# Performance work log

Measured on AMD Instinct MI355X. Metric: run time of the kernel, lower is better.

Reference implementation:

```python
import jax, jax.numpy as jnp
import numpy as np

N, H, W, C = 8, 64, 64, 256  # C//4 = 64 query channels, HW = 4096 attention size


def setup_inputs() -> dict:
    key = jax.random.key(0)
    k1, k2, k3, k4 = jax.random.split(key, 4)
    src_mask = jax.random.uniform(k1, (N, H, W), dtype=jnp.float32)
    src_feature = jax.random.normal(k2, (N, H, W, C), dtype=jnp.float32)
    ref_feature = jax.random.normal(k3, (N, H, W, C), dtype=jnp.float32)
    w_query = jax.random.normal(k4, (C, C // 4), dtype=jnp.float32) * 0.02  # 1x1 conv weight
    return {"src_mask": src_mask, "src_feature": src_feature,
            "ref_feature": ref_feature, "w_query": w_query}


def _apply_attention_map(att_map, features):
    n, h, w, c = features.shape
    pixels = features.reshape(n, h * w, c).transpose(0, 2, 1)  # (N, C, HW)
    att_out = jnp.einsum('ncp,npq->ncq', pixels, att_map)      # (N, C, HW)
    return att_out.reshape(n, h, w, c)


def reference(src_mask, src_feature, ref_feature, w_query):
    n, h, w, c = src_feature.shape
    # 1x1 conv (no bias): per-pixel channel projection C -> C//4
    query = jnp.einsum('nhwc,cd->nhwd', src_feature, w_query).reshape(n, h * w, -1)
    # full (HW x HW) attention map, softmax over keys
    att_map = jax.nn.softmax(jnp.einsum('npd,nqd->npq', query, query), axis=-1)
    # original module applies the map to src_feature twice (src_att and ref_att)
    att_out = _apply_attention_map(att_map, src_feature)
    src_att = att_out
    ref_att = att_out
    m = src_mask[..., None]  # (N, H, W, 1)
    ex_guide_flow = m * ref_att + (1.0 - m) * ref_feature
    return jnp.concatenate([ex_guide_flow, src_att], axis=-1)  # (N, H, W, 2C)
```

## Files before the change

kernel.cpp:

```cpp
#include <hip/hip_runtime.h>

typedef unsigned short u16;
typedef unsigned int u32;
typedef __attribute__((ext_vector_type(8))) __bf16 bf16x8;
typedef __attribute__((ext_vector_type(8))) _Float16 f16x8;
typedef __attribute__((ext_vector_type(4))) float f32x4;

__device__ __forceinline__ float b2f(u16 b) {
    union { u32 u; float f; } v; v.u = ((u32)b) << 16; return v.f;
}
__device__ __forceinline__ u16 f2bf(float f) {
    union { float f; u32 u; } v; v.f = f;
    u32 u = v.u;
    return (u16)((u + 0x7fffu + ((u >> 16) & 1u)) >> 16);
}
__device__ __forceinline__ u16 f2h(float f) {
    _Float16 h = (_Float16)f;
    return __builtin_bit_cast(u16, h);
}
__device__ __forceinline__ u32 pkbf2(float a, float b) {
    u16 x = __builtin_bit_cast(u16, (__bf16)a);
    u16 y = __builtin_bit_cast(u16, (__bf16)b);
    return (u32)x | ((u32)y << 16);
}
__device__ __forceinline__ bf16x8 ldg8b(const u16* p) {
    uint4 v = *(const uint4*)p;
    return __builtin_bit_cast(bf16x8, v);
}
__device__ __forceinline__ f16x8 ldg8h(const u16* p) {
    uint4 v = *(const uint4*)p;
    return __builtin_bit_cast(f16x8, v);
}
__device__ __forceinline__ f32x4 mfma_bf(bf16x8 a, bf16x8 b, f32x4 c) {
    return __builtin_amdgcn_mfma_f32_16x16x32_bf16(a, b, c, 0, 0, 0);
}
__device__ __forceinline__ f32x4 mfma_h(f16x8 a, f16x8 b, f32x4 c) {
    return __builtin_amdgcn_mfma_f32_16x16x32_f16(a, b, c, 0, 0, 0);
}
__device__ __forceinline__ void gld16(const u16* g, u16* l) {
    __builtin_amdgcn_global_load_lds(
        (const __attribute__((address_space(1))) u32*)g,
        (__attribute__((address_space(3))) u32*)l, 16, 0, 0);
}

#define LOG2E 1.44269504088896340736f


__global__ void k0_wt(const float* __restrict__ Wq,
                      u16* __restrict__ Wthi, u16* __restrict__ Wtlo) {
    int idx = blockIdx.x * 256 + threadIdx.x;
    int c = idx >> 6, d = idx & 63;
    float w = Wq[idx];
    u16 hi = f2bf(w);
    float rem = w - b2f(hi);
    Wthi[d * 256 + c] = hi;
    Wtlo[d * 256 + c] = f2bf(rem);
}

__global__ __launch_bounds__(256) void k1_query(
    const float* __restrict__ F, const u16* __restrict__ Wthi,
    const u16* __restrict__ Wtlo, u16* __restrict__ Qh) {
    const int t = threadIdx.x;
    const int w = t >> 6, L = t & 63, lane16 = L & 15, quad = L >> 4;
    const int R0 = blockIdx.x * 64;
    const int row = R0 + w * 16 + lane16;
    const f32x4 z4 = {0.f, 0.f, 0.f, 0.f};
    f32x4 acc[4] = {z4, z4, z4, z4};
    union U8 { bf16x8 v; u16 s[8]; };
#pragma unroll
    for (int ks = 0; ks < 8; ++ks) {
        const float* fp = F + (size_t)row * 256 + ks * 32 + quad * 8;
        float4 x0 = *(const float4*)fp;
        float4 x1 = *(const float4*)(fp + 4);
        float xs[8] = {x0.x, x0.y, x0.z, x0.w, x1.x, x1.y, x1.z, x1.w};
        U8 ahi, alo;
#pragma unroll
        for (int j = 0; j < 8; ++j) {
            u16 h = f2bf(xs[j]);
            ahi.s[j] = h;
            alo.s[j] = f2bf(xs[j] - b2f(h));
        }
#pragma unroll
        for (int nt = 0; nt < 4; ++nt) {
            const int off = (nt * 16 + lane16) * 256 + ks * 32 + quad * 8;
            bf16x8 bh = ldg8b(Wthi + off);
            bf16x8 bl = ldg8b(Wtlo + off);
            acc[nt] = mfma_bf(ahi.v, bh, acc[nt]);
            acc[nt] = mfma_bf(alo.v, bh, acc[nt]);
            acc[nt] = mfma_bf(ahi.v, bl, acc[nt]);
        }
    }
    const int orow = R0 + w * 16 + quad * 4;
#pragma unroll
    for (int nt = 0; nt < 4; ++nt) {
        const int d = nt * 16 + lane16;
#pragma unroll
        for (int r = 0; r < 4; ++r) {
            const int p = orow + r;
            Qh[(size_t)p * 64 + (d ^ ((p & 7) << 3))] = f2h(acc[nt][r]);
        }
    }
}

__global__ __launch_bounds__(256) void k2_suminv(
    const u16* __restrict__ Q, float* __restrict__ lgl) {
    const int t = threadIdx.x;
    const int w = t >> 6, L = t & 63, lane16 = L & 15, quad = L >> 4, l7 = lane16 & 7;
    const int bx = blockIdx.x;
    const int n = bx & 7, pb = bx >> 3;
    const int P0 = pb * 32;
    const u16* Qn = Q + (size_t)n * 4096 * 64;

    f16x8 ap[2][2];
#pragma unroll
    for (int st = 0; st < 2; ++st) {
        const int row = P0 + st * 16 + lane16;
        ap[st][0] = ldg8h(Qn + row * 64 + ((quad * 8) ^ (l7 * 8)));
        ap[st][1] = ldg8h(Qn + row * 64 + ((32 + quad * 8) ^ (l7 * 8)));
    }
    float sums[2][4];
#pragma unroll
    for (int st = 0; st < 2; ++st)
#pragma unroll
        for (int r = 0; r < 4; ++r) sums[st][r] = 0.f;

    const f32x4 z4 = {0.f, 0.f, 0.f, 0.f};
    for (int s = 0; s < 32; ++s) {
#pragma unroll
        for (int nt = 0; nt < 2; ++nt) {
            const int qr = w * 1024 + s * 32 + nt * 16 + lane16;
            f16x8 b0 = ldg8h(Qn + qr * 64 + ((quad * 8) ^ (l7 * 8)));
            f16x8 b1 = ldg8h(Qn + qr * 64 + ((32 + quad * 8) ^ (l7 * 8)));
#pragma unroll
            for (int st = 0; st < 2; ++st) {
                f32x4 z = z4;
                z = mfma_h(ap[st][0], b0, z);
                z = mfma_h(ap[st][1], b1, z);
                sums[st][0] += __expf(z[0]);
                sums[st][1] += __expf(z[1]);
                sums[st][2] += __expf(z[2]);
                sums[st][3] += __expf(z[3]);
            }
        }
    }
    __shared__ float red[4][32];
#pragma unroll
    for (int st = 0; st < 2; ++st)
#pragma unroll
        for (int r = 0; r < 4; ++r) {
            float v = sums[st][r];
            v += __shfl_xor(v, 1);
            v += __shfl_xor(v, 2);
            v += __shfl_xor(v, 4);
            v += __shfl_xor(v, 8);
            if (lane16 == 0) red[w][st * 16 + quad * 4 + r] = v;
        }
    __syncthreads();
    if (t < 32) {
        float tot = red[0][t] + red[1][t] + red[2][t] + red[3][t];
        lgl[n * 4096 + P0 + t] = -__log2f(tot);
    }
}

__global__ __launch_bounds__(256) void k3_gt(
    const float* __restrict__ F, u16* __restrict__ Gt) {
    const int t = threadIdx.x;
    const int bx = blockIdx.x;
    const int n = bx >> 6, s = bx & 63;
    const int p0 = s * 64;
    __shared__ float tile[64][65];
    const float* Fn = F + (size_t)n * 4096 * 256;
    u16* Gn = Gt + (size_t)(n * 64 + s) * 16384;
#pragma unroll 1
    for (int ct = 0; ct < 4; ++ct) {
        const int c0 = ct * 64;
        if (ct > 0) __syncthreads();
#pragma unroll
        for (int k = 0; k < 16; ++k) {
            int idx = k * 256 + t;
            int r = idx >> 6, cc = idx & 63;
            tile[r][cc] = Fn[(size_t)(p0 + r) * 256 + c0 + cc];
        }
        __syncthreads();
#pragma unroll
        for (int k = 0; k < 2; ++k) {
            int u = k * 256 + t;
            int cc = u & 63, S = u >> 6;
            int G = S ^ (cc & 7);
            u16 v[8];
#pragma unroll
            for (int j = 0; j < 8; ++j) v[j] = f2bf(tile[G * 8 + j][cc]);
            uint4 pk;
            pk.x = (u32)v[0] | ((u32)v[1] << 16);
            pk.y = (u32)v[2] | ((u32)v[3] << 16);
            pk.z = (u32)v[4] | ((u32)v[5] << 16);
            pk.w = (u32)v[6] | ((u32)v[7] << 16);
            *(uint4*)&Gn[(c0 + cc) * 64 + S * 8] = pk;
        }
    }
}

__global__ __launch_bounds__(256, 2) void k4_attn(
    const u16* __restrict__ Q, const u16* __restrict__ Gt,
    const float* __restrict__ lgl, const float* __restrict__ mask,
    const float* __restrict__ ref, float* __restrict__ out) {
    const int t = threadIdx.x;
    const int w = t >> 6, L = t & 63, lane16 = L & 15, quad = L >> 4, l7 = lane16 & 7;
    const int bx = blockIdx.x;
    const int n = bx & 7, qb = bx >> 3;
    const int q0 = qb << 6;

    __shared__ u16 sGt[2][16384];
    __shared__ u16 sP[2][4096];

    const u16* Qn = Q + (size_t)n * 4096 * 64;
    const u16* Gtn = Gt + (size_t)n * 64 * 16384;
    const float* iln = lgl + n * 4096;

    f16x8 bq[4][2];
#pragma unroll
    for (int qt = 0; qt < 4; ++qt) {
        const int row = q0 + qt * 16 + lane16;
        bq[qt][0] = ldg8h(Qn + row * 64 + ((quad * 8) ^ (l7 * 8)));
        bq[qt][1] = ldg8h(Qn + row * 64 + ((32 + quad * 8) ^ (l7 * 8)));
    }

    const int sAg0 = (w * 16 + lane16) * 64 + ((quad * 8) ^ (l7 * 8));
    const int sAg1 = (w * 16 + lane16) * 64 + ((32 + quad * 8) ^ (l7 * 8));
    int wrP[4];
#pragma unroll
    for (int qt = 0; qt < 4; ++qt)
        wrP[qt] = (qt * 16 + lane16) * 64 +
                  ((w * 16 + 8 * (quad >> 1)) ^ (l7 * 8)) + 4 * (quad & 1);
    int rdP[4][2], sOf[4][2];
#pragma unroll
    for (int m = 0; m < 4; ++m)
#pragma unroll
        for (int h = 0; h < 2; ++h)
            rdP[m][h] = (m * 16 + lane16) * 64 + ((h * 32 + quad * 8) ^ (l7 * 8));
#pragma unroll
    for (int nt = 0; nt < 4; ++nt)
#pragma unroll
        for (int h = 0; h < 2; ++h)
            sOf[nt][h] = (w * 64 + nt * 16 + lane16) * 64 + ((h * 32 + quad * 8) ^ (l7 * 8));
    const int dl = L * 8;

    const f32x4 z4 = {0.f, 0.f, 0.f, 0.f};
    f32x4 acc[4][4];
#pragma unroll
    for (int a = 0; a < 4; ++a)
#pragma unroll
        for (int b = 0; b < 4; ++b) acc[a][b] = z4;

    {
        f16x8 a0 = ldg8h(Qn + sAg0);
        f16x8 a1 = ldg8h(Qn + sAg1);
        float4 il4 = *(const float4*)(iln + w * 16 + quad * 4);
        float lg[4] = {il4.x, il4.y, il4.z, il4.w};
#pragma unroll
        for (int qt = 0; qt < 4; ++qt) {
            f32x4 z = z4;
            z = mfma_h(a0, bq[qt][0], z);
            z = mfma_h(a1, bq[qt][1], z);
            uint2 pk;
            pk.x = pkbf2(__builtin_exp2f(__builtin_fmaf(z[0], LOG2E, lg[0])),
                         __builtin_exp2f(__builtin_fmaf(z[1], LOG2E, lg[1])));
            pk.y = pkbf2(__builtin_exp2f(__builtin_fmaf(z[2], LOG2E, lg[2])),
                         __builtin_exp2f(__builtin_fmaf(z[3], LOG2E, lg[3])));
            *(uint2*)&sP[0][wrP[qt]] = pk;
        }
    }
    __builtin_amdgcn_sched_barrier(0);
#pragma unroll
    for (int j = 0; j < 8; ++j) {
        const int c = w * 8 + j;
        gld16(Gtn + c * 512 + dl, &sGt[0][c * 512]);
    }
    __builtin_amdgcn_sched_barrier(0);
    f16x8 na0 = ldg8h(Qn + 4096 + sAg0);
    f16x8 na1 = ldg8h(Qn + 4096 + sAg1);
    float4 nil4 = *(const float4*)(iln + 64 + w * 16 + quad * 4);
    __builtin_amdgcn_sched_barrier(0);
    asm volatile("s_waitcnt lgkmcnt(0)" ::: "memory");
    __builtin_amdgcn_s_barrier();

#pragma unroll 1
    for (int i = 0; i < 64; ++i) {
        const int cur = i & 1, nxt = cur ^ 1;
        if (i + 1 < 64) {
            float lg[4] = {nil4.x, nil4.y, nil4.z, nil4.w};
#pragma unroll
            for (int qt = 0; qt < 4; ++qt) {
                f32x4 z = z4;
                z = mfma_h(na0, bq[qt][0], z);
                z = mfma_h(na1, bq[qt][1], z);
                uint2 pk;
                pk.x = pkbf2(__builtin_exp2f(__builtin_fmaf(z[0], LOG2E, lg[0])),
                             __builtin_exp2f(__builtin_fmaf(z[1], LOG2E, lg[1])));
                pk.y = pkbf2(__builtin_exp2f(__builtin_fmaf(z[2], LOG2E, lg[2])),
                             __builtin_exp2f(__builtin_fmaf(z[3], LOG2E, lg[3])));
                *(uint2*)&sP[nxt][wrP[qt]] = pk;
            }
            __builtin_amdgcn_sched_barrier(0);
            const u16* gsrc = Gtn + (size_t)(i + 1) * 16384;
#pragma unroll
            for (int j = 0; j < 8; ++j) {
                const int c = w * 8 + j;
                gld16(gsrc + c * 512 + dl, &sGt[nxt][c * 512]);
            }
            __builtin_amdgcn_sched_barrier(0);
            if (i + 2 < 64) {
                na0 = ldg8h(Qn + (size_t)(i + 2) * 4096 + sAg0);
                na1 = ldg8h(Qn + (size_t)(i + 2) * 4096 + sAg1);
                nil4 = *(const float4*)(iln + (i + 2) * 64 + w * 16 + quad * 4);
            }
            __builtin_amdgcn_sched_barrier(0);
        } else {
            asm volatile("s_waitcnt vmcnt(0)" ::: "memory");
        }
#pragma unroll
        for (int h = 0; h < 2; ++h) {
            bf16x8 af[4], bb[4];
#pragma unroll
            for (int m = 0; m < 4; ++m) af[m] = ldg8b(&sP[cur][rdP[m][h]]);
#pragma unroll
            for (int nt = 0; nt < 4; ++nt) bb[nt] = ldg8b(&sGt[cur][sOf[nt][h]]);
#pragma unroll
            for (int nt = 0; nt < 4; ++nt)
#pragma unroll
                for (int m = 0; m < 4; ++m)
                    acc[m][nt] = mfma_bf(af[m], bb[nt], acc[m][nt]);
        }
        asm volatile("s_waitcnt lgkmcnt(0)" ::: "memory");
        __builtin_amdgcn_s_barrier();
    }

    const int tb = qb >> 2;
    const int cb = (qb & 3) * 64;
    const float* maskn = mask + n * 4096;
    const float* refn = ref + (size_t)n * 4096 * 256;
    float* outn = out + (size_t)n * 4096 * 512;
#pragma unroll
    for (int nt = 0; nt < 4; ++nt) {
        const int ch = w * 64 + nt * 16 + lane16;
        const int pixel = ch * 16 + tb;
        const float m = maskn[pixel];
#pragma unroll
        for (int mt = 0; mt < 4; ++mt) {
            const int c4 = cb + mt * 16 + quad * 4;
            float4 r4 = *(const float4*)(refn + (size_t)pixel * 256 + c4);
            float a0 = acc[mt][nt][0], a1 = acc[mt][nt][1];
            float a2 = acc[mt][nt][2], a3 = acc[mt][nt][3];
            float4 a4 = {a0, a1, a2, a3};
            float4 bl4 = {m * a0 + (1.f - m) * r4.x,
                          m * a1 + (1.f - m) * r4.y,
                          m * a2 + (1.f - m) * r4.z,
                          m * a3 + (1.f - m) * r4.w};
            *(float4*)(outn + (size_t)pixel * 512 + 256 + c4) = a4;
            *(float4*)(outn + (size_t)pixel * 512 + c4) = bl4;
        }
    }
}

extern "C" void kernel_launch(void* const* d_in, const int* in_sizes, int n_in,
                              void* d_out, int out_size, void* d_ws, size_t ws_size,
                              hipStream_t stream) {
    const float* mask = (const float*)d_in[0];
    const float* F    = (const float*)d_in[1];
    const float* ref  = (const float*)d_in[2];
    const float* Wq   = (const float*)d_in[3];
    float* out = (float*)d_out;
    char* ws = (char*)d_ws;

    u16*   Wthi = (u16*)ws;
    u16*   Wtlo = (u16*)(ws + 32768);
    u16*   Qh   = (u16*)(ws + 65536);
    float* lgl  = (float*)(ws + 65536 + 4194304);
    u16*   Gt   = (u16*)(ws + 65536 + 4194304 + 131072);

    k0_wt    <<<64,   256, 0, stream>>>(Wq, Wthi, Wtlo);
    k1_query <<<512,  256, 0, stream>>>(F, Wthi, Wtlo, Qh);
    k2_suminv<<<1024, 256, 0, stream>>>(Qh, lgl);
    k3_gt    <<<512,  256, 0, stream>>>(F, Gt);
    k4_attn  <<<512,  256, 0, stream>>>(Qh, Gt, lgl, mask, ref, out);
}
```

Before: 286.5 us.

## Load value tiles directly from global into registers, dropping LDS staging

Removes the shared-memory buffer for the Gt (value) tiles. Each wave now reads its B-fragments straight from global memory into two register sets, double-buffered across a loop unrolled by two. The loop also raises wave priority around the PV MFMA phase with s_setprio. The goal is to cut LDS capacity and LDS read traffic so occupancy can rise. In exchange each wave issues more scattered global loads and holds extra registers, and any load latency the pipeline fails to hide becomes a stall.

```diff
diff --git a/kernel.cpp b/kernel.cpp
--- a/kernel.cpp
+++ b/kernel.cpp
@@ -36,11 +36,6 @@
 }
 __device__ __forceinline__ f32x4 mfma_h(f16x8 a, f16x8 b, f32x4 c) {
     return __builtin_amdgcn_mfma_f32_16x16x32_f16(a, b, c, 0, 0, 0);
-}
-__device__ __forceinline__ void gld16(const u16* g, u16* l) {
-    __builtin_amdgcn_global_load_lds(
-        (const __attribute__((address_space(1))) u32*)g,
-        (__attribute__((address_space(3))) u32*)l, 16, 0, 0);
 }
 
 #define LOG2E 1.44269504088896340736f
@@ -210,7 +205,6 @@
     const int n = bx & 7, qb = bx >> 3;
     const int q0 = qb << 6;
 
-    __shared__ u16 sGt[2][16384];
     __shared__ u16 sP[2][4096];
 
     const u16* Qn = Q + (size_t)n * 4096 * 64;
@@ -243,7 +237,6 @@
 #pragma unroll
         for (int h = 0; h < 2; ++h)
             sOf[nt][h] = (w * 64 + nt * 16 + lane16) * 64 + ((h * 32 + quad * 8) ^ (l7 * 8));
-    const int dl = L * 8;
 
     const f32x4 z4 = {0.f, 0.f, 0.f, 0.f};
     f32x4 acc[4][4];
@@ -252,85 +245,94 @@
 #pragma unroll
         for (int b = 0; b < 4; ++b) acc[a][b] = z4;
 
-    {
-        f16x8 a0 = ldg8h(Qn + sAg0);
-        f16x8 a1 = ldg8h(Qn + sAg1);
-        float4 il4 = *(const float4*)(iln + w * 16 + quad * 4);
-        float lg[4] = {il4.x, il4.y, il4.z, il4.w};
+    f16x8 na0, na1;
+    float4 nil4;
+    bf16x8 bbA[8], bbB[8];
+
+    auto s_phase = [&](f16x8 a0, f16x8 a1, float4 il4, u16* dst) {
+        float lg0 = il4.x, lg1 = il4.y, lg2 = il4.z, lg3 = il4.w;
 #pragma unroll
         for (int qt = 0; qt < 4; ++qt) {
             f32x4 z = z4;
             z = mfma_h(a0, bq[qt][0], z);
             z = mfma_h(a1, bq[qt][1], z);
             uint2 pk;
-            pk.x = pkbf2(__builtin_exp2f(__builtin_fmaf(z[0], LOG2E, lg[0])),
-                         __builtin_exp2f(__builtin_fmaf(z[1], LOG2E, lg[1])));
-            pk.y = pkbf2(__builtin_exp2f(__builtin_fmaf(z[2], LOG2E, lg[2])),
-                         __builtin_exp2f(__builtin_fmaf(z[3], LOG2E, lg[3])));
-            *(uint2*)&sP[0][wrP[qt]] = pk;
-        }
+            pk.x = pkbf2(__builtin_exp2f(__builtin_fmaf(z[0], LOG2E, lg0)),
+                         __builtin_exp2f(__builtin_fmaf(z[1], LOG2E, lg1)));
+            pk.y = pkbf2(__builtin_exp2f(__builtin_fmaf(z[2], LOG2E, lg2)),
+                         __builtin_exp2f(__builtin_fmaf(z[3], LOG2E, lg3)));
+            *(uint2*)&dst[wrP[qt]] = pk;
+        }
+    };
+    auto load_bb = [&](const u16* gstep, bf16x8* bb) {
+#pragma unroll
+        for (int h = 0; h < 2; ++h)
+#pragma unroll
+            for (int nt = 0; nt < 4; ++nt)
+                bb[h * 4 + nt] = ldg8b(gstep + sOf[nt][h]);
+    };
+    auto pv_phase = [&](const u16* sPc, const bf16x8* bb) {
+        __builtin_amdgcn_s_setprio(1);
+#pragma unroll
+        for (int h = 0; h < 2; ++h) {
+            bf16x8 af[4];
+#pragma unroll
+            for (int m = 0; m < 4; ++m) af[m] = ldg8b(&sPc[rdP[m][h]]);
+#pragma unroll
+            for (int nt = 0; nt < 4; ++nt)
+#pragma unroll
+                for (int m = 0; m < 4; ++m)
+                    acc[m][nt] = mfma_bf(af[m], bb[h * 4 + nt], acc[m][nt]);
+        }
+        __builtin_amdgcn_s_setprio(0);
+    };
+
+    {
+        f16x8 a0 = ldg8h(Qn + sAg0);
+        f16x8 a1 = ldg8h(Qn + sAg1);
+        float4 il4 = *(const float4*)(iln + w * 16 + quad * 4);
+        s_phase(a0, a1, il4, &sP[0][0]);
     }
     __builtin_amdgcn_sched_barrier(0);
-#pragma unroll
-    for (int j = 0; j < 8; ++j) {
-        const int c = w * 8 + j;
-        gld16(Gtn + c * 512 + dl, &sGt[0][c * 512]);
-    }
+    na0 = ldg8h(Qn + 4096 + sAg0);
+    na1 = ldg8h(Qn + 4096 + sAg1);
+    nil4 = *(const float4*)(iln + 64 + w * 16 + quad * 4);
     __builtin_amdgcn_sched_barrier(0);
-    f16x8 na0 = ldg8h(Qn + 4096 + sAg0);
-    f16x8 na1 = ldg8h(Qn + 4096 + sAg1);
-    float4 nil4 = *(const float4*)(iln + 64 + w * 16 + quad * 4);
+    load_bb(Gtn, bbA);
     __builtin_amdgcn_sched_barrier(0);
     asm volatile("s_waitcnt lgkmcnt(0)" ::: "memory");
     __builtin_amdgcn_s_barrier();
 
 #pragma unroll 1
-    for (int i = 0; i < 64; ++i) {
-        const int cur = i & 1, nxt = cur ^ 1;
-        if (i + 1 < 64) {
-            float lg[4] = {nil4.x, nil4.y, nil4.z, nil4.w};
-#pragma unroll
-            for (int qt = 0; qt < 4; ++qt) {
-                f32x4 z = z4;
-                z = mfma_h(na0, bq[qt][0], z);
-                z = mfma_h(na1, bq[qt][1], z);
-                uint2 pk;
-                pk.x = pkbf2(__builtin_exp2f(__builtin_fmaf(z[0], LOG2E, lg[0])),
-                             __builtin_exp2f(__builtin_fmaf(z[1], LOG2E, lg[1])));
-                pk.y = pkbf2(__builtin_exp2f(__builtin_fmaf(z[2], LOG2E, lg[2])),
-                             __builtin_exp2f(__builtin_fmaf(z[3], LOG2E, lg[3])));
-                *(uint2*)&sP[nxt][wrP[qt]] = pk;
+    for (int j = 0; j < 32; ++j) {
+        const int i = 2 * j;
+        s_phase(na0, na1, nil4, &sP[1][0]);
+        __builtin_amdgcn_sched_barrier(0);
+        if (i + 2 < 64) {
+            na0 = ldg8h(Qn + (size_t)(i + 2) * 4096 + sAg0);
+            na1 = ldg8h(Qn + (size_t)(i + 2) * 4096 + sAg1);
+            nil4 = *(const float4*)(iln + (i + 2) * 64 + w * 16 + quad * 4);
+        }
+        __builtin_amdgcn_sched_barrier(0);
+        load_bb(Gtn + (size_t)(i + 1) * 16384, bbB);
+        __builtin_amdgcn_sched_barrier(0);
+        pv_phase(&sP[0][0], bbA);
+        asm volatile("s_waitcnt lgkmcnt(0)" ::: "memory");
+        __builtin_amdgcn_s_barrier();
+
+        if (i + 2 < 64) {
+            s_phase(na0, na1, nil4, &sP[0][0]);
+            __builtin_amdgcn_sched_barrier(0);
+            if (i + 3 < 64) {
+                na0 = ldg8h(Qn + (size_t)(i + 3) * 4096 + sAg0);
+                na1 = ldg8h(Qn + (size_t)(i + 3) * 4096 + sAg1);
+                nil4 = *(const float4*)(iln + (i + 3) * 64 + w * 16 + quad * 4);
             }
             __builtin_amdgcn_sched_barrier(0);
-            const u16* gsrc = Gtn + (size_t)(i + 1) * 16384;
-#pragma unroll
-            for (int j = 0; j < 8; ++j) {
-                const int c = w * 8 + j;
-                gld16(gsrc + c * 512 + dl, &sGt[nxt][c * 512]);
-            }
+            load_bb(Gtn + (size_t)(i + 2) * 16384, bbA);
             __builtin_amdgcn_sched_barrier(0);
-            if (i + 2 < 64) {
-                na0 = ldg8h(Qn + (size_t)(i + 2) * 4096 + sAg0);
-                na1 = ldg8h(Qn + (size_t)(i + 2) * 4096 + sAg1);
-                nil4 = *(const float4*)(iln + (i + 2) * 64 + w * 16 + quad * 4);
-            }
-            __builtin_amdgcn_sched_barrier(0);
-        } else {
-            asm volatile("s_waitcnt vmcnt(0)" ::: "memory");
-        }
-#pragma unroll
-        for (int h = 0; h < 2; ++h) {
-            bf16x8 af[4], bb[4];
-#pragma unroll
-            for (int m = 0; m < 4; ++m) af[m] = ldg8b(&sP[cur][rdP[m][h]]);
-#pragma unroll
-            for (int nt = 0; nt < 4; ++nt) bb[nt] = ldg8b(&sGt[cur][sOf[nt][h]]);
-#pragma unroll
-            for (int nt = 0; nt < 4; ++nt)
-#pragma unroll
-                for (int m = 0; m < 4; ++m)
-                    acc[m][nt] = mfma_bf(af[m], bb[nt], acc[m][nt]);
-        }
+        }
+        pv_phase(&sP[1][0], bbB);
         asm volatile("s_waitcnt lgkmcnt(0)" ::: "memory");
         __builtin_amdgcn_s_barrier();
     }
```

Measured after the change: 279.2 us. 2.5% less time.
